# Performance work log

Hardware: AMD Instinct MI355X
Metric: run time of the kernel (lower is better)

## Reference

```python
import jax, jax.numpy as jnp
import numpy as np

N, E, G = 20000, 200000, 32
D, H, C, L = 384, 12, 32, 6
NUM_RBF = 100
RBF_MIN, RBF_MAX = 0.0, 30.0


def _layer_norm(x, g, b, eps=1e-5):
    mu = jnp.mean(x, axis=-1, keepdims=True)
    var = jnp.var(x, axis=-1, keepdims=True)
    return (x - mu) * jax.lax.rsqrt(var + eps) * g + b


def setup_inputs() -> dict:
    key = jax.random.key(0)
    ks = jax.random.split(key, 32)
    s = 0.05
    inp = {
        'x': jax.random.normal(ks[0], (N, 20), jnp.float32),
        'pos': jax.random.normal(ks[1], (N, 3), jnp.float32) * 10.0,
        'edge_index': jax.random.randint(ks[2], (2, E), 0, N),
        'batch': jnp.sort(jax.random.randint(ks[3], (N,), 0, G)),
        # node embedding: Linear(20,384) + LayerNorm
        'emb_W': jax.random.normal(ks[4], (20, D)) * s,
        'emb_b': jnp.zeros((D,)),
        'emb_g': jnp.ones((D,)),
        'emb_beta': jnp.zeros((D,)),
        # edge encoder: Linear(100,384), Linear(384,384), LayerNorm
        'eW1': jax.random.normal(ks[5], (NUM_RBF, D)) * s,
        'eb1': jnp.zeros((D,)),
        'eW2': jax.random.normal(ks[6], (D, D)) * s,
        'eb2': jnp.zeros((D,)),
        'e_g': jnp.ones((D,)),
        'e_beta': jnp.zeros((D,)),
        # 6 stacked GATv2 layers
        'Wl': jax.random.normal(ks[7], (L, D, D)) * s,
        'bl': jnp.zeros((L, D)),
        'Wr': jax.random.normal(ks[8], (L, D, D)) * s,
        'br': jnp.zeros((L, D)),
        'We': jax.random.normal(ks[9], (L, D, D)) * s,
        'att': jax.random.normal(ks[10], (L, H, C)) * s,
        'cb': jnp.zeros((L, D)),
        # BatchNorm (eval mode, running stats)
        'bn_g': 1.0 + jax.random.normal(ks[11], (L, D)) * 0.05,
        'bn_b': jax.random.normal(ks[12], (L, D)) * 0.05,
        'bn_m': jax.random.normal(ks[13], (L, D)) * 0.05,
        'bn_v': jax.random.uniform(ks[14], (L, D), minval=0.5, maxval=1.5),
        # pool combine + head
        'pW': jax.random.normal(ks[15], (2 * D, D)) * s,
        'pb': jnp.zeros((D,)),
        'hW1': jax.random.normal(ks[16], (D, D)) * s,
        'hb1': jnp.zeros((D,)),
        'hW2': jax.random.normal(ks[17], (D, D // 2)) * s,
        'hb2': jnp.zeros((D // 2,)),
        'hW3': jax.random.normal(ks[18], (D // 2, 1)) * s,
        'hb3': jnp.zeros((1,)),
    }
    return inp


def reference(x, pos, edge_index, batch, emb_W, emb_b, emb_g, emb_beta,
              eW1, eb1, eW2, eb2, e_g, e_beta,
              Wl, bl, Wr, br, We, att, cb, bn_g, bn_b, bn_m, bn_v,
              pW, pb, hW1, hb1, hW2, hb2, hW3, hb3):
    src, dst = edge_index[0], edge_index[1]

    # node embedding (dropout = identity in eval)
    h = jax.nn.silu(_layer_norm(x @ emb_W + emb_b, emb_g, emb_beta))  # (N, D)

    # RBF edge features
    centers = jnp.linspace(RBF_MIN, RBF_MAX, NUM_RBF)
    spacing = (RBF_MAX - RBF_MIN) / (NUM_RBF - 1)
    gamma = 1.0 / (spacing ** 2 + 1e-8)
    dist = jnp.linalg.norm(pos[src] - pos[dst], axis=-1, keepdims=True)  # (E, 1)
    rbf = jnp.exp(-gamma * (dist - centers) ** 2)  # (E, NUM_RBF)
    e = jax.nn.silu(rbf @ eW1 + eb1)
    e = _layer_norm(e @ eW2 + eb2, e_g, e_beta)  # (E, D)

    for i in range(L):
        identity = h
        xl = (h @ Wl[i] + bl[i]).reshape(N, H, C)
        xr = (h @ Wr[i] + br[i]).reshape(N, H, C)
        ee = (e @ We[i]).reshape(E, H, C)
        m = jax.nn.leaky_relu(xl[src] + xr[dst] + ee, 0.2)  # (E, H, C)
        logits = jnp.einsum('ehc,hc->eh', m, att[i])  # (E, H)
        smax = jax.ops.segment_max(logits, dst, num_segments=N)
        a = jnp.exp(logits - smax[dst])
        denom = jax.ops.segment_sum(a, dst, num_segments=N)
        a = a / (denom[dst] + 1e-16)
        msg = (xl[src] * a[:, :, None]).reshape(E, H * C)
        out = jax.ops.segment_sum(msg, dst, num_segments=N) + cb[i]  # (N, D)
        out = (out - bn_m[i]) * jax.lax.rsqrt(bn_v[i] + 1e-5) * bn_g[i] + bn_b[i]
        h = jax.nn.silu(out) + identity

    cnt = jax.ops.segment_sum(jnp.ones((N,), h.dtype), batch, num_segments=G)
    h_mean = jax.ops.segment_sum(h, batch, num_segments=G) / jnp.maximum(cnt, 1.0)[:, None]
    h_max = jax.ops.segment_max(h, batch, num_segments=G)
    hg = jnp.concatenate([h_mean, h_max], axis=-1)  # (G, 2D)
    hg = jax.nn.silu(hg @ pW + pb)
    hg = jax.nn.silu(hg @ hW1 + hb1)
    hg = jax.nn.silu(hg @ hW2 + hb2)
    return (hg @ hW3 + hb3).squeeze(-1)  # (G,)
```

## Files before the change

kernel.cpp:

```cpp
#include <hip/hip_runtime.h>
#include <hip/hip_bf16.h>
#include <math.h>

#define NN 20000
#define EE 200000
#define GG 32
#define DD 384
#define HH 12
#define CC 32
#define LL 6
#define NRBF 100
#define CHUNK 32768

typedef short s16x8 __attribute__((ext_vector_type(8)));
typedef float f32x4 __attribute__((ext_vector_type(4)));
typedef unsigned int u32;

__device__ __forceinline__ float siluf(float x) { return x / (1.f + __expf(-x)); }
__device__ __forceinline__ float bf2f(unsigned short u) {
    return __uint_as_float(((unsigned int)u) << 16);
}

__device__ __forceinline__ void atomicMaxF(float* addr, float val) {
    if (val >= 0.f) atomicMax((int*)addr, __float_as_int(val));
    else atomicMin((unsigned int*)addr, __float_as_uint(val));
}

__device__ __forceinline__ void gload16(const void* g, void* l) {
    __builtin_amdgcn_global_load_lds((const __attribute__((address_space(1))) u32*)g,
                                     (__attribute__((address_space(3))) u32*)l, 16, 0, 0);
}

__device__ __forceinline__ bool tile_decode(int NC, int nrows, int& rowt, int& col) {
    const int t = blockIdx.x;
    const int q = t >> 3;
    col = q % NC;
    rowt = (q / NC) * 8 + (t & 7);
    return rowt < nrows;
}

__global__ void EquivariantProteinGNN_45552423141948_kernel() {}

__device__ __forceinline__ void gemm_kloop(const __hip_bfloat16* __restrict__ A,
                                           const __hip_bfloat16* __restrict__ Bt,
                                           int M, int K, int m0, int n0,
                                           unsigned short* As, unsigned short* Bs,
                                           f32x4 (&acc)[4][4]) {
    char* AsB = (char*)As;
    char* BsB = (char*)Bs;
    const int t = threadIdx.x;
    const int w = t >> 6, l = t & 63;
    const int wr = w >> 1, wc = w & 1;

    const int s0 = 4 * w;
    size_t aS[4], bS[4];
#pragma unroll
    for (int i = 0; i < 4; ++i) {
        const int s = s0 + i;
        const int row = s * 8 + (l >> 3);
        const int cg = (l & 7) ^ (row & 7);
        aS[i] = (size_t)min(m0 + row, M - 1) * K + cg * 8;
        bS[i] = (size_t)(n0 + row) * K + cg * 8;
    }

    int aoff[2][4], boff[2][4];
#pragma unroll
    for (int sub = 0; sub < 2; ++sub)
#pragma unroll
        for (int m = 0; m < 4; ++m) {
            const int row = wr * 64 + m * 16 + (l & 15);
            aoff[sub][m] = row * 128 + ((((l >> 4) + 4 * sub) ^ (row & 7)) << 4);
            const int rowb = wc * 64 + m * 16 + (l & 15);
            boff[sub][m] = rowb * 128 + ((((l >> 4) + 4 * sub) ^ (rowb & 7)) << 4);
        }

    for (int kk = 0; kk < K; kk += 64) {
        __syncthreads();
#pragma unroll
        for (int i = 0; i < 4; ++i) gload16(A + aS[i] + kk, As + (s0 + i) * 512);
#pragma unroll
        for (int i = 0; i < 4; ++i) gload16(Bt + bS[i] + kk, Bs + (s0 + i) * 512);
        __syncthreads();
#pragma unroll
        for (int sub = 0; sub < 2; ++sub) {
            s16x8 af[4], bfr[4];
#pragma unroll
            for (int m = 0; m < 4; ++m) af[m] = *(const s16x8*)(AsB + aoff[sub][m]);
#pragma unroll
            for (int n = 0; n < 4; ++n) bfr[n] = *(const s16x8*)(BsB + boff[sub][n]);
#pragma unroll
            for (int m = 0; m < 4; ++m)
#pragma unroll
                for (int n = 0; n < 4; ++n)
                    acc[m][n] = __builtin_amdgcn_mfma_f32_16x16x32_bf16(af[m], bfr[n],
                                                                        acc[m][n], 0, 0, 0);
        }
    }
}

template<bool BIAS, bool SILU>
__global__ __launch_bounds__(256) void k_gemm_bt(const __hip_bfloat16* __restrict__ A,
                                                 const __hip_bfloat16* __restrict__ Bt,
                                                 const float* __restrict__ bias,
                                                 __hip_bfloat16* __restrict__ Cmat,
                                                 int M, int N, int K) {
    int rowt, colt;
    if (!tile_decode(N >> 7, (M + 127) >> 7, rowt, colt)) return;
    const int m0 = rowt << 7, n0 = colt << 7;

    __shared__ unsigned short As[128 * 64];
    __shared__ unsigned short Bs[128 * 64];
    const int l = threadIdx.x & 63;
    const int w = threadIdx.x >> 6;
    const int wr = w >> 1, wc = w & 1;

    f32x4 acc[4][4] = {};
    gemm_kloop(A, Bt, M, K, m0, n0, As, Bs, acc);

#pragma unroll
    for (int n = 0; n < 4; ++n) {
        const int col = n0 + wc * 64 + n * 16 + (l & 15);
        const float bv = BIAS ? bias[col] : 0.f;
#pragma unroll
        for (int m = 0; m < 4; ++m) {
            const int rbase = m0 + wr * 64 + m * 16 + ((l >> 4) << 2);
#pragma unroll
            for (int r = 0; r < 4; ++r) {
                const int row = rbase + r;
                if (row < M) {
                    float v = acc[m][n][r] + bv;
                    if (SILU) v = siluf(v);
                    Cmat[(size_t)row * N + col] = __float2bfloat16(v);
                }
            }
        }
    }
}

__global__ __launch_bounds__(256) void k_gemm_attn(const __hip_bfloat16* __restrict__ A,
                                                   const __hip_bfloat16* __restrict__ Bt,
                                                   const __hip_bfloat16* __restrict__ xlr,
                                                   const int* __restrict__ src_p,
                                                   const int* __restrict__ dst_p,
                                                   const float* __restrict__ att_i,
                                                   float* __restrict__ logits,
                                                   int M, int K) {
    int rowt, colt;
    if (!tile_decode(DD >> 7, (M + 127) >> 7, rowt, colt)) return;
    const int m0 = rowt << 7, n0 = colt << 7;

    __shared__ char smem[32768];
    unsigned short* As = (unsigned short*)smem;
    unsigned short* Bs = (unsigned short*)(smem + 16384);
    const int l = threadIdx.x & 63;
    const int w = threadIdx.x >> 6;
    const int wr = w >> 1, wc = w & 1;

    f32x4 acc[4][4] = {};
    gemm_kloop(A, Bt, M, K, m0, n0, As, Bs, acc);

    __syncthreads();

    float* ep = (float*)(smem + w * 4096);
    const int row_l = l >> 2;
    const int c0 = (l & 3) << 4;
    const int gcol = n0 + wc * 64 + c0;
    const int hbase = (n0 + wc * 64) >> 5;
    const int rswz = row_l << 2;

    float attv[16];
#pragma unroll
    for (int k = 0; k < 4; ++k)
        *(float4*)(attv + 4 * k) = *(const float4*)(att_i + gcol + 4 * k);

#pragma unroll
    for (int m = 0; m < 4; ++m) {
#pragma unroll
        for (int n = 0; n < 4; ++n)
#pragma unroll
            for (int r = 0; r < 4; ++r) {
                const int row = ((l >> 4) << 2) + r;
                const int col = (n << 4) + (l & 15);
                ep[(row << 6) + (col ^ (row << 2))] = acc[m][n][r];
            }
        const int growu = m0 + wr * 64 + m * 16 + row_l;
        const int grow = min(growu, M - 1);
        const int s = src_p[grow], d = dst_p[grow];
        float av[16];
#pragma unroll
        for (int k = 0; k < 4; ++k) {
            const int sc0 = (c0 + (k << 2)) ^ rswz;
            *(f32x4*)(av + 4 * k) = *(const f32x4*)(ep + (row_l << 6) + sc0);
        }
        const uint4 vl0 = *(const uint4*)(xlr + (size_t)s * 768 + gcol);
        const uint4 vl1 = *(const uint4*)(xlr + (size_t)s * 768 + gcol + 8);
        const uint4 vr0 = *(const uint4*)(xlr + (size_t)d * 768 + 384 + gcol);
        const uint4 vr1 = *(const uint4*)(xlr + (size_t)d * 768 + 384 + gcol + 8);
        const u32 lw[8] = {vl0.x, vl0.y, vl0.z, vl0.w, vl1.x, vl1.y, vl1.z, vl1.w};
        const u32 rw[8] = {vr0.x, vr0.y, vr0.z, vr0.w, vr1.x, vr1.y, vr1.z, vr1.w};
        float part = 0.f;
#pragma unroll
        for (int q = 0; q < 8; ++q) {
            float v0 = av[2 * q] + bf2f((unsigned short)(lw[q] & 0xffff)) +
                       bf2f((unsigned short)(rw[q] & 0xffff));
            float v1 = av[2 * q + 1] + bf2f((unsigned short)(lw[q] >> 16)) +
                       bf2f((unsigned short)(rw[q] >> 16));
            v0 = (v0 > 0.f) ? v0 : 0.2f * v0;
            v1 = (v1 > 0.f) ? v1 : 0.2f * v1;
            part += v0 * attv[2 * q] + v1 * attv[2 * q + 1];
        }
        part += __shfl_xor(part, 1, 64);
        if (growu < M && (l & 1) == 0)
            logits[(size_t)growu * HH + hbase + ((l & 2) >> 1)] = part;
    }
}

__global__ void k_tw(const float* __restrict__ in, __hip_bfloat16* __restrict__ out, int nmat) {
    const size_t idx = (size_t)blockIdx.x * 256 + threadIdx.x;
    if (idx >= (size_t)nmat * DD * DD) return;
    const int m = idx / (DD * DD);
    const int rem = idx - (size_t)m * DD * DD;
    const int n = rem / DD, k = rem - n * DD;
    out[idx] = __float2bfloat16(in[(size_t)m * DD * DD + (size_t)k * DD + n]);
}

__global__ void k_twlr(const float* __restrict__ Wl, const float* __restrict__ Wr,
                       __hip_bfloat16* __restrict__ out) {
    const size_t idx = (size_t)blockIdx.x * 256 + threadIdx.x;
    if (idx >= (size_t)LL * 768 * DD) return;
    const int i = idx / (768 * DD);
    const int rem = idx - (size_t)i * 768 * DD;
    const int n = rem / DD, k = rem - n * DD;
    const float v = (n < DD) ? Wl[(size_t)i * DD * DD + (size_t)k * DD + n]
                             : Wr[(size_t)i * DD * DD + (size_t)k * DD + (n - DD)];
    out[idx] = __float2bfloat16(v);
}

__global__ void k_blr(const float* __restrict__ bl, const float* __restrict__ br,
                      float* __restrict__ blr) {
    const int idx = blockIdx.x * 256 + threadIdx.x;
    if (idx >= LL * 768) return;
    const int i = idx / 768, c = idx - i * 768;
    blr[idx] = (c < DD) ? bl[i * DD + c] : br[i * DD + c - DD];
}

__global__ void k_tw1(const float* __restrict__ in, __hip_bfloat16* __restrict__ out) {
    const int idx = blockIdx.x * 256 + threadIdx.x;
    if (idx >= DD * 128) return;
    const int n = idx >> 7, k = idx & 127;
    out[idx] = __float2bfloat16(k < NRBF ? in[(size_t)k * DD + n] : 0.f);
}

__global__ __launch_bounds__(256) void k_rbf_chunk(const float* __restrict__ pos,
                                                   const int* __restrict__ src_p,
                                                   const int* __restrict__ dst_p,
                                                   int e0, int cm,
                                                   __hip_bfloat16* __restrict__ rbfp) {
    const int el = blockIdx.x * 2 + (threadIdx.x >> 7);
    if (el >= cm) return;
    const int e = e0 + el;
    const int c = threadIdx.x & 127;
    const int s = src_p[e], d = dst_p[e];
    const float dx = pos[s * 3 + 0] - pos[d * 3 + 0];
    const float dy = pos[s * 3 + 1] - pos[d * 3 + 1];
    const float dz = pos[s * 3 + 2] - pos[d * 3 + 2];
    const float dist = sqrtf(dx * dx + dy * dy + dz * dz);
    const float spacing = 30.f / 99.f;
    const float gamma = 1.f / (spacing * spacing + 1e-8f);
    float v = 0.f;
    if (c < NRBF) {
        const float dd = dist - (float)c * spacing;
        v = __expf(-gamma * dd * dd);
    }
    rbfp[(size_t)el * 128 + c] = __float2bfloat16(v);
}

__global__ __launch_bounds__(512) void k_ln_rows(__hip_bfloat16* __restrict__ u,
                                                 const float* __restrict__ g,
                                                 const float* __restrict__ be) {
    const int w = threadIdx.x >> 6, l = threadIdx.x & 63;
    const int row = blockIdx.x * 8 + w;
    float vals[8];
    float s = 0.f, q = 0.f;
    if (l < 48) {
        const uint4 vu = *(const uint4*)(u + (size_t)row * DD + 8 * l);
        const unsigned int* uw = (const unsigned int*)&vu;
#pragma unroll
        for (int i = 0; i < 4; ++i) {
            vals[2 * i] = bf2f((unsigned short)(uw[i] & 0xffff));
            vals[2 * i + 1] = bf2f((unsigned short)(uw[i] >> 16));
        }
#pragma unroll
        for (int i = 0; i < 8; ++i) { s += vals[i]; q += vals[i] * vals[i]; }
    }
#pragma unroll
    for (int off = 1; off < 64; off <<= 1) {
        s += __shfl_xor(s, off, 64);
        q += __shfl_xor(q, off, 64);
    }
    const float mu = s / DD;
    const float rs = rsqrtf(q / DD - mu * mu + 1e-5f);
    if (l < 48) {
        unsigned int ow[4];
        const float4 g0 = *(const float4*)(g + 8 * l);
        const float4 g1 = *(const float4*)(g + 8 * l + 4);
        const float4 b0 = *(const float4*)(be + 8 * l);
        const float4 b1 = *(const float4*)(be + 8 * l + 4);
        const float gv[8] = {g0.x, g0.y, g0.z, g0.w, g1.x, g1.y, g1.z, g1.w};
        const float bv[8] = {b0.x, b0.y, b0.z, b0.w, b1.x, b1.y, b1.z, b1.w};
#pragma unroll
        for (int i = 0; i < 4; ++i) {
            const float y0 = (vals[2 * i] - mu) * rs * gv[2 * i] + bv[2 * i];
            const float y1 = (vals[2 * i + 1] - mu) * rs * gv[2 * i + 1] + bv[2 * i + 1];
            const unsigned short h0 = __bfloat16_as_ushort(__float2bfloat16(y0));
            const unsigned short h1 = __bfloat16_as_ushort(__float2bfloat16(y1));
            ow[i] = (unsigned int)h0 | ((unsigned int)h1 << 16);
        }
        *(uint4*)(u + (size_t)row * DD + 8 * l) = *(uint4*)ow;
    }
}

__global__ __launch_bounds__(384) void k_node_embed(const float* __restrict__ x,
                                                    const float* __restrict__ W,
                                                    const float* __restrict__ b,
                                                    const float* __restrict__ g,
                                                    const float* __restrict__ be,
                                                    float* __restrict__ h,
                                                    __hip_bfloat16* __restrict__ hb) {
    const int n = blockIdx.x, j = threadIdx.x;
    __shared__ float xrow[20];
    __shared__ float red[12];
    if (j < 20) xrow[j] = x[n * 20 + j];
    __syncthreads();
    float acc = b[j];
#pragma unroll
    for (int k = 0; k < 20; ++k) acc += xrow[k] * W[k * DD + j];
    float s = acc, q = acc * acc;
#pragma unroll
    for (int off = 32; off > 0; off >>= 1) {
        s += __shfl_down(s, off, 64);
        q += __shfl_down(q, off, 64);
    }
    const int wid = j >> 6;
    if ((j & 63) == 0) { red[wid] = s; red[6 + wid] = q; }
    __syncthreads();
    if (j == 0) {
        float ts = 0.f, tq = 0.f;
        for (int w = 0; w < 6; ++w) { ts += red[w]; tq += red[6 + w]; }
        float mu = ts / DD;
        red[0] = mu; red[6] = tq / DD - mu * mu;
    }
    __syncthreads();
    const float mu = red[0], var = red[6];
    float y = (acc - mu) * rsqrtf(var + 1e-5f) * g[j] + be[j];
    y = siluf(y);
    h[(size_t)n * DD + j] = y;
    hb[(size_t)n * DD + j] = __float2bfloat16(y);
}

__global__ void k_deg(const int* __restrict__ ei, int* __restrict__ deg) {
    int e = blockIdx.x * blockDim.x + threadIdx.x;
    if (e < EE) atomicAdd(&deg[ei[EE + e]], 1);
}

__global__ __launch_bounds__(1024) void k_scan(const int* __restrict__ deg, int* __restrict__ rp) {
    __shared__ int buf[1024];
    __shared__ int carry_s;
    const int tid = threadIdx.x;
    if (tid == 0) carry_s = 0;
    __syncthreads();
    for (int base = 0; base < NN; base += 1024) {
        int v = (base + tid < NN) ? deg[base + tid] : 0;
        buf[tid] = v;
        __syncthreads();
        for (int off = 1; off < 1024; off <<= 1) {
            int t = (tid >= off) ? buf[tid - off] : 0;
            __syncthreads();
            buf[tid] += t;
            __syncthreads();
        }
        const int incl = buf[tid];
        const int carry = carry_s;
        if (base + tid < NN) rp[base + tid] = carry + incl - v;
        __syncthreads();
        if (tid == 1023) carry_s = carry + incl;
        __syncthreads();
    }
    if (tid == 0) rp[NN] = carry_s;
}

__global__ void k_scatter(const int* __restrict__ ei, const int* __restrict__ rp,
                          int* __restrict__ cursor, int* __restrict__ col_e) {
    int e = blockIdx.x * blockDim.x + threadIdx.x;
    if (e < EE) {
        int d = ei[EE + e];
        int p = atomicAdd(&cursor[d], 1);
        col_e[rp[d] + p] = e;
    }
}

__global__ void k_perm(const int* __restrict__ ei, const int* __restrict__ col_e,
                       int* __restrict__ src_p, int* __restrict__ dst_p) {
    int p = blockIdx.x * blockDim.x + threadIdx.x;
    if (p < EE) {
        const int e = col_e[p];
        src_p[p] = ei[e];
        dst_p[p] = ei[EE + e];
    }
}

__global__ __launch_bounds__(256) void k_node_aggr(const float* __restrict__ logits,
                                                   const __hip_bfloat16* __restrict__ xlr,
                                                   const int* __restrict__ src_p,
                                                   const int* __restrict__ rp,
                                                   const float* __restrict__ cb_i,
                                                   const float* __restrict__ g_i,
                                                   const float* __restrict__ b_i,
                                                   const float* __restrict__ m_i,
                                                   const float* __restrict__ v_i,
                                                   float* __restrict__ h,
                                                   __hip_bfloat16* __restrict__ hb) {
    const int wv = threadIdx.x >> 6, l = threadIdx.x & 63;
    const int n = blockIdx.x * 4 + wv;
    if (n >= NN) return;
    const int beg = rp[n], end = rp[n + 1];

    float mx = -INFINITY, sum = 0.f;
    if (l < HH) {
        for (int i = beg; i < end; ++i) mx = fmaxf(mx, logits[(size_t)i * HH + l]);
        for (int i = beg; i < end; ++i) sum += __expf(logits[(size_t)i * HH + l] - mx);
    }
    const int head = (l < 48) ? (l >> 2) : 0;
    const float m_h = __shfl(mx, head, 64);
    const float inv_h = 1.f / (__shfl(sum, head, 64) + 1e-16f);

    if (l >= 48) return;
    const int c0 = l * 8;
    float acc[8] = {};
    for (int i = beg; i < end; ++i) {
        const float a = __expf(logits[(size_t)i * HH + head] - m_h) * inv_h;
        const int s = src_p[i];
        const uint4 vx = *(const uint4*)(xlr + (size_t)s * 768 + c0);
        const u32* xw = (const u32*)&vx;
#pragma unroll
        for (int q = 0; q < 4; ++q) {
            acc[2 * q]     += bf2f((unsigned short)(xw[q] & 0xffff)) * a;
            acc[2 * q + 1] += bf2f((unsigned short)(xw[q] >> 16)) * a;
        }
    }
    const float4 cb0 = *(const float4*)(cb_i + c0), cb1 = *(const float4*)(cb_i + c0 + 4);
    const float4 gg0 = *(const float4*)(g_i + c0),  gg1 = *(const float4*)(g_i + c0 + 4);
    const float4 bb0 = *(const float4*)(b_i + c0),  bb1 = *(const float4*)(b_i + c0 + 4);
    const float4 mm0 = *(const float4*)(m_i + c0),  mm1 = *(const float4*)(m_i + c0 + 4);
    const float4 vv0 = *(const float4*)(v_i + c0),  vv1 = *(const float4*)(v_i + c0 + 4);
    const float cbv[8] = {cb0.x, cb0.y, cb0.z, cb0.w, cb1.x, cb1.y, cb1.z, cb1.w};
    const float gv[8]  = {gg0.x, gg0.y, gg0.z, gg0.w, gg1.x, gg1.y, gg1.z, gg1.w};
    const float bv[8]  = {bb0.x, bb0.y, bb0.z, bb0.w, bb1.x, bb1.y, bb1.z, bb1.w};
    const float mv[8]  = {mm0.x, mm0.y, mm0.z, mm0.w, mm1.x, mm1.y, mm1.z, mm1.w};
    const float vvv[8] = {vv0.x, vv0.y, vv0.z, vv0.w, vv1.x, vv1.y, vv1.z, vv1.w};
    float4 h0 = *(const float4*)(h + (size_t)n * DD + c0);
    float4 h1 = *(const float4*)(h + (size_t)n * DD + c0 + 4);
    float hv[8] = {h0.x, h0.y, h0.z, h0.w, h1.x, h1.y, h1.z, h1.w};
    unsigned int ow[4];
#pragma unroll
    for (int q = 0; q < 8; ++q) {
        float o = acc[q] + cbv[q];
        o = (o - mv[q]) * rsqrtf(vvv[q] + 1e-5f) * gv[q] + bv[q];
        hv[q] = siluf(o) + hv[q];
    }
#pragma unroll
    for (int q = 0; q < 4; ++q) {
        const unsigned short b0 = __bfloat16_as_ushort(__float2bfloat16(hv[2 * q]));
        const unsigned short b1 = __bfloat16_as_ushort(__float2bfloat16(hv[2 * q + 1]));
        ow[q] = (unsigned int)b0 | ((unsigned int)b1 << 16);
    }
    *(float4*)(h + (size_t)n * DD + c0) = make_float4(hv[0], hv[1], hv[2], hv[3]);
    *(float4*)(h + (size_t)n * DD + c0 + 4) = make_float4(hv[4], hv[5], hv[6], hv[7]);
    *(uint4*)(hb + (size_t)n * DD + c0) = *(uint4*)ow;
}

__global__ void k_fill(float* __restrict__ p, float v, int n) {
    int i = blockIdx.x * blockDim.x + threadIdx.x;
    if (i < n) p[i] = v;
}

__global__ __launch_bounds__(384) void k_pool2(const float* __restrict__ h,
                                               const int* __restrict__ batch,
                                               float* __restrict__ gsum,
                                               float* __restrict__ gmax,
                                               float* __restrict__ gcnt) {
    const int j = threadIdx.x;
    const int n0 = blockIdx.x * 256;
    const int n1 = min(n0 + 256, NN);
    int cur = batch[n0];
    float s = 0.f, mx = -INFINITY;
    int cnt = 0;
    for (int n = n0; n < n1; ++n) {
        const int g = batch[n];
        if (g != cur) {
            atomicAdd(&gsum[cur * DD + j], s);
            atomicMaxF(&gmax[cur * DD + j], mx);
            if (j == 0) atomicAdd(&gcnt[cur], (float)cnt);
            s = 0.f; mx = -INFINITY; cnt = 0; cur = g;
        }
        const float v = h[(size_t)n * DD + j];
        s += v; mx = fmaxf(mx, v); ++cnt;
    }
    atomicAdd(&gsum[cur * DD + j], s);
    atomicMaxF(&gmax[cur * DD + j], mx);
    if (j == 0) atomicAdd(&gcnt[cur], (float)cnt);
}

__global__ __launch_bounds__(384) void k_head(const float* __restrict__ gsum,
                                              const float* __restrict__ gmax,
                                              const float* __restrict__ gcnt,
                                              const float* __restrict__ pW,
                                              const float* __restrict__ pb,
                                              const float* __restrict__ hW1,
                                              const float* __restrict__ hb1,
                                              const float* __restrict__ hW2,
                                              const float* __restrict__ hb2,
                                              const float* __restrict__ hW3,
                                              const float* __restrict__ hb3,
                                              float* __restrict__ out) {
    const int g = blockIdx.x, j = threadIdx.x;
    __shared__ float hg[2 * DD];
    __shared__ float p1[DD];
    __shared__ float p2[DD];
    __shared__ float p3[DD / 2];
    __shared__ float red[6];
    const float cnt = fmaxf(gcnt[g], 1.f);
    hg[j] = gsum[g * DD + j] / cnt;
    hg[DD + j] = gmax[g * DD + j];
    __syncthreads();
    float a = pb[j];
    for (int k = 0; k < 2 * DD; ++k) a += hg[k] * pW[(size_t)k * DD + j];
    p1[j] = siluf(a);
    __syncthreads();
    a = hb1[j];
    for (int k = 0; k < DD; ++k) a += p1[k] * hW1[(size_t)k * DD + j];
    p2[j] = siluf(a);
    __syncthreads();
    if (j < DD / 2) {
        a = hb2[j];
        for (int k = 0; k < DD; ++k) a += p2[k] * hW2[(size_t)k * (DD / 2) + j];
        p3[j] = siluf(a);
    }
    __syncthreads();
    float v = (j < DD / 2) ? p3[j] * hW3[j] : 0.f;
#pragma unroll
    for (int off = 32; off > 0; off >>= 1) v += __shfl_down(v, off, 64);
    if ((j & 63) == 0) red[j >> 6] = v;
    __syncthreads();
    if (j == 0) {
        float s = 0.f;
        for (int w = 0; w < 6; ++w) s += red[w];
        out[g] = s + hb3[0];
    }
}

static inline int gemm_grid(int M, int N) {
    const int nr = (M + 127) >> 7, nc = N >> 7;
    return ((nr + 7) >> 3) * nc * 8;
}

extern "C" void kernel_launch(void* const* d_in, const int* in_sizes, int n_in,
                              void* d_out, int out_size, void* d_ws, size_t ws_size,
                              hipStream_t stream) {
    (void)in_sizes; (void)n_in; (void)out_size; (void)ws_size;
    const float* x      = (const float*)d_in[0];
    const float* pos    = (const float*)d_in[1];
    const int*   ei     = (const int*)d_in[2];
    const int*   batch  = (const int*)d_in[3];
    const float* emb_W  = (const float*)d_in[4];
    const float* emb_b  = (const float*)d_in[5];
    const float* emb_g  = (const float*)d_in[6];
    const float* emb_be = (const float*)d_in[7];
    const float* eW1    = (const float*)d_in[8];
    const float* eb1    = (const float*)d_in[9];
    const float* eW2    = (const float*)d_in[10];
    const float* eb2    = (const float*)d_in[11];
    const float* e_g    = (const float*)d_in[12];
    const float* e_be   = (const float*)d_in[13];
    const float* Wl     = (const float*)d_in[14];
    const float* bl     = (const float*)d_in[15];
    const float* Wr     = (const float*)d_in[16];
    const float* br     = (const float*)d_in[17];
    const float* We     = (const float*)d_in[18];
    const float* att    = (const float*)d_in[19];
    const float* cb     = (const float*)d_in[20];
    const float* bn_g   = (const float*)d_in[21];
    const float* bn_b   = (const float*)d_in[22];
    const float* bn_m   = (const float*)d_in[23];
    const float* bn_v   = (const float*)d_in[24];
    const float* pW     = (const float*)d_in[25];
    const float* pb     = (const float*)d_in[26];
    const float* hW1    = (const float*)d_in[27];
    const float* hb1    = (const float*)d_in[28];
    const float* hW2    = (const float*)d_in[29];
    const float* hb2    = (const float*)d_in[30];
    const float* hW3    = (const float*)d_in[31];
    const float* hb3    = (const float*)d_in[32];

    char* wp = (char*)d_ws;
    auto carve = [&](size_t bytes) -> void* {
        void* p = (void*)wp;
        wp += (bytes + 255) & ~(size_t)255;
        return p;
    };
    float* h      = (float*)carve((size_t)NN * DD * 4);
    __hip_bfloat16* hbf = (__hip_bfloat16*)carve((size_t)NN * DD * 2);
    __hip_bfloat16* xlr = (__hip_bfloat16*)carve((size_t)NN * 768 * 2);
    __hip_bfloat16* ebf = (__hip_bfloat16*)carve((size_t)EE * DD * 2);
    float* logits = (float*)carve((size_t)EE * HH * 4);
    int* deg      = (int*)carve((size_t)NN * 4);
    int* cursor   = (int*)carve((size_t)NN * 4);
    int* rp       = (int*)carve((size_t)(NN + 1) * 4);
    int* col_e    = (int*)carve((size_t)EE * 4);
    int* src_p    = (int*)carve((size_t)EE * 4);
    int* dst_p    = (int*)carve((size_t)EE * 4);
    float* gsum   = (float*)carve((size_t)GG * DD * 4);
    float* gmax   = (float*)carve((size_t)GG * DD * 4);
    float* gcnt   = (float*)carve((size_t)GG * 4);
    __hip_bfloat16* Wlrt = (__hip_bfloat16*)carve((size_t)LL * 768 * DD * 2);
    __hip_bfloat16* Wet  = (__hip_bfloat16*)carve((size_t)LL * DD * DD * 2);
    float* blr    = (float*)carve((size_t)LL * 768 * 4);
    __hip_bfloat16* eW1t = (__hip_bfloat16*)carve((size_t)DD * 128 * 2);
    __hip_bfloat16* eW2t = (__hip_bfloat16*)carve((size_t)DD * DD * 2);

    __hip_bfloat16* rbfc = (__hip_bfloat16*)logits;
    __hip_bfloat16* tc   = xlr;

    hipMemsetAsync(deg, 0, (size_t)NN * 4, stream);
    hipMemsetAsync(cursor, 0, (size_t)NN * 4, stream);

    {
        const int nblkLR = (int)(((size_t)LL * 768 * DD + 255) / 256);
        const int nblk6 = (int)(((size_t)LL * DD * DD + 255) / 256);
        k_twlr<<<nblkLR, 256, 0, stream>>>(Wl, Wr, Wlrt);
        k_tw<<<nblk6, 256, 0, stream>>>(We, Wet, LL);
        k_blr<<<(LL * 768 + 255) / 256, 256, 0, stream>>>(bl, br, blr);
        k_tw<<<(DD * DD + 255) / 256, 256, 0, stream>>>(eW2, eW2t, 1);
        k_tw1<<<(DD * 128 + 255) / 256, 256, 0, stream>>>(eW1, eW1t);
    }

    k_node_embed<<<NN, 384, 0, stream>>>(x, emb_W, emb_b, emb_g, emb_be, h, hbf);

    k_deg<<<(EE + 255) / 256, 256, 0, stream>>>(ei, deg);
    k_scan<<<1, 1024, 0, stream>>>(deg, rp);
    k_scatter<<<(EE + 255) / 256, 256, 0, stream>>>(ei, rp, cursor, col_e);
    k_perm<<<(EE + 255) / 256, 256, 0, stream>>>(ei, col_e, src_p, dst_p);

    for (int c0 = 0; c0 < EE; c0 += CHUNK) {
        const int cm = (EE - c0 < CHUNK) ? (EE - c0) : CHUNK;
        k_rbf_chunk<<<(cm + 1) / 2, 256, 0, stream>>>(pos, src_p, dst_p, c0, cm, rbfc);
        k_gemm_bt<true, true><<<gemm_grid(cm, DD), 256, 0, stream>>>(rbfc, eW1t, eb1, tc, cm, DD, 128);
        k_gemm_bt<true, false><<<gemm_grid(cm, DD), 256, 0, stream>>>(tc, eW2t, eb2,
                                                                      ebf + (size_t)c0 * DD, cm, DD, DD);
    }
    k_ln_rows<<<EE / 8, 512, 0, stream>>>(ebf, e_g, e_be);

    for (int i = 0; i < LL; ++i) {
        const __hip_bfloat16* Wlrt_i = Wlrt + (size_t)i * 768 * DD;
        const __hip_bfloat16* Wet_i  = Wet + (size_t)i * DD * DD;
        const float* blr_i = blr + (size_t)i * 768;
        const float* att_i = att + (size_t)i * HH * CC;
        const float* cb_i  = cb + (size_t)i * DD;
        const float* bng_i = bn_g + (size_t)i * DD;
        const float* bnb_i = bn_b + (size_t)i * DD;
        const float* bnm_i = bn_m + (size_t)i * DD;
        const float* bnv_i = bn_v + (size_t)i * DD;

        k_gemm_bt<true, false><<<gemm_grid(NN, 768), 256, 0, stream>>>(hbf, Wlrt_i, blr_i, xlr,
                                                                       NN, 768, DD);
        k_gemm_attn<<<gemm_grid(EE, DD), 256, 0, stream>>>(ebf, Wet_i, xlr, src_p, dst_p,
                                                           att_i, logits, EE, DD);
        k_node_aggr<<<(NN + 3) / 4, 256, 0, stream>>>(logits, xlr, src_p, rp, cb_i, bng_i, bnb_i,
                                                      bnm_i, bnv_i, h, hbf);
    }

    hipMemsetAsync(gsum, 0, (size_t)GG * DD * 4, stream);
    hipMemsetAsync(gcnt, 0, (size_t)GG * 4, stream);
    k_fill<<<(GG * DD + 255) / 256, 256, 0, stream>>>(gmax, -INFINITY, GG * DD);
    k_pool2<<<(NN + 255) / 256, 384, 0, stream>>>(h, batch, gsum, gmax, gcnt);
    k_head<<<GG, 384, 0, stream>>>(gsum, gmax, gcnt, pW, pb, hW1, hb1, hW2, hb2, hW3, hb3,
                                   (float*)d_out);
}
```

Baseline: 1.884 ms.

## Halve GEMM K-tile to 32 with new LDS swizzle and hoist epilogue gathers

Shrinks the per-block LDS tiles from 128x64 to 128x32 bf16, with a matching XOR swizzle and one MFMA sub-step per iteration. This halves shared memory use, which can allow more resident blocks. In the attention-fused GEMM, the src/dst index and xl/xr gather loads are issued before the LDS transpose to hide their latency. The trade-off is twice as many barrier-separated K iterations, with less work per sync.

```diff
diff --git a/kernel.cpp b/kernel.cpp
--- a/kernel.cpp
+++ b/kernel.cpp
@@ -52,49 +52,46 @@
     const int w = t >> 6, l = t & 63;
     const int wr = w >> 1, wc = w & 1;
 
-    const int s0 = 4 * w;
-    size_t aS[4], bS[4];
-#pragma unroll
-    for (int i = 0; i < 4; ++i) {
-        const int s = s0 + i;
-        const int row = s * 8 + (l >> 3);
-        const int cg = (l & 7) ^ (row & 7);
-        aS[i] = (size_t)min(m0 + row, M - 1) * K + cg * 8;
-        bS[i] = (size_t)(n0 + row) * K + cg * 8;
-    }
-
-    int aoff[2][4], boff[2][4];
-#pragma unroll
-    for (int sub = 0; sub < 2; ++sub)
-#pragma unroll
-        for (int m = 0; m < 4; ++m) {
-            const int row = wr * 64 + m * 16 + (l & 15);
-            aoff[sub][m] = row * 128 + ((((l >> 4) + 4 * sub) ^ (row & 7)) << 4);
-            const int rowb = wc * 64 + m * 16 + (l & 15);
-            boff[sub][m] = rowb * 128 + ((((l >> 4) + 4 * sub) ^ (rowb & 7)) << 4);
-        }
-
-    for (int kk = 0; kk < K; kk += 64) {
+    const int seg0 = 2 * w, seg1 = seg0 + 1;
+    const int r0s = seg0 * 16 + (l >> 2);
+    const int r1s = seg1 * 16 + (l >> 2);
+    const int cg0 = (l & 3) ^ ((r0s >> 1) & 3);
+    const int cg1 = (l & 3) ^ ((r1s >> 1) & 3);
+    const size_t aSrc0 = (size_t)min(m0 + r0s, M - 1) * K + cg0 * 8;
+    const size_t aSrc1 = (size_t)min(m0 + r1s, M - 1) * K + cg1 * 8;
+    const size_t bSrc0 = (size_t)(n0 + r0s) * K + cg0 * 8;
+    const size_t bSrc1 = (size_t)(n0 + r1s) * K + cg1 * 8;
+    unsigned short* AsW0 = As + seg0 * 512;
+    unsigned short* AsW1 = As + seg1 * 512;
+    unsigned short* BsW0 = Bs + seg0 * 512;
+    unsigned short* BsW1 = Bs + seg1 * 512;
+
+    int aoff[4], boff[4];
+#pragma unroll
+    for (int m = 0; m < 4; ++m) {
+        const int row = wr * 64 + m * 16 + (l & 15);
+        aoff[m] = row * 64 + ((((l >> 4)) ^ ((row >> 1) & 3)) << 4);
+        const int rowb = wc * 64 + m * 16 + (l & 15);
+        boff[m] = rowb * 64 + ((((l >> 4)) ^ ((rowb >> 1) & 3)) << 4);
+    }
+
+    for (int kk = 0; kk < K; kk += 32) {
         __syncthreads();
-#pragma unroll
-        for (int i = 0; i < 4; ++i) gload16(A + aS[i] + kk, As + (s0 + i) * 512);
-#pragma unroll
-        for (int i = 0; i < 4; ++i) gload16(Bt + bS[i] + kk, Bs + (s0 + i) * 512);
+        gload16(A + aSrc0 + kk, AsW0);
+        gload16(A + aSrc1 + kk, AsW1);
+        gload16(Bt + bSrc0 + kk, BsW0);
+        gload16(Bt + bSrc1 + kk, BsW1);
         __syncthreads();
-#pragma unroll
-        for (int sub = 0; sub < 2; ++sub) {
-            s16x8 af[4], bfr[4];
-#pragma unroll
-            for (int m = 0; m < 4; ++m) af[m] = *(const s16x8*)(AsB + aoff[sub][m]);
-#pragma unroll
-            for (int n = 0; n < 4; ++n) bfr[n] = *(const s16x8*)(BsB + boff[sub][n]);
-#pragma unroll
-            for (int m = 0; m < 4; ++m)
-#pragma unroll
-                for (int n = 0; n < 4; ++n)
-                    acc[m][n] = __builtin_amdgcn_mfma_f32_16x16x32_bf16(af[m], bfr[n],
-                                                                        acc[m][n], 0, 0, 0);
-        }
+        s16x8 af[4], bfr[4];
+#pragma unroll
+        for (int m = 0; m < 4; ++m) af[m] = *(const s16x8*)(AsB + aoff[m]);
+#pragma unroll
+        for (int n = 0; n < 4; ++n) bfr[n] = *(const s16x8*)(BsB + boff[n]);
+#pragma unroll
+        for (int m = 0; m < 4; ++m)
+#pragma unroll
+            for (int n = 0; n < 4; ++n)
+                acc[m][n] = __builtin_amdgcn_mfma_f32_16x16x32_bf16(af[m], bfr[n], acc[m][n], 0, 0, 0);
     }
 }
 
@@ -108,8 +105,8 @@
     if (!tile_decode(N >> 7, (M + 127) >> 7, rowt, colt)) return;
     const int m0 = rowt << 7, n0 = colt << 7;
 
-    __shared__ unsigned short As[128 * 64];
-    __shared__ unsigned short Bs[128 * 64];
+    __shared__ unsigned short As[128 * 32];
+    __shared__ unsigned short Bs[128 * 32];
     const int l = threadIdx.x & 63;
     const int w = threadIdx.x >> 6;
     const int wr = w >> 1, wc = w & 1;
@@ -149,9 +146,9 @@
     if (!tile_decode(DD >> 7, (M + 127) >> 7, rowt, colt)) return;
     const int m0 = rowt << 7, n0 = colt << 7;
 
-    __shared__ char smem[32768];
+    __shared__ char smem[16384];
     unsigned short* As = (unsigned short*)smem;
-    unsigned short* Bs = (unsigned short*)(smem + 16384);
+    unsigned short* Bs = (unsigned short*)(smem + 8192);
     const int l = threadIdx.x & 63;
     const int w = threadIdx.x >> 6;
     const int wr = w >> 1, wc = w & 1;
@@ -175,6 +172,14 @@
 
 #pragma unroll
     for (int m = 0; m < 4; ++m) {
+        const int growu = m0 + wr * 64 + m * 16 + row_l;
+        const int grow = min(growu, M - 1);
+        const int s = src_p[grow], d = dst_p[grow];
+        const uint4 vl0 = *(const uint4*)(xlr + (size_t)s * 768 + gcol);
+        const uint4 vl1 = *(const uint4*)(xlr + (size_t)s * 768 + gcol + 8);
+        const uint4 vr0 = *(const uint4*)(xlr + (size_t)d * 768 + 384 + gcol);
+        const uint4 vr1 = *(const uint4*)(xlr + (size_t)d * 768 + 384 + gcol + 8);
+
 #pragma unroll
         for (int n = 0; n < 4; ++n)
 #pragma unroll
@@ -183,19 +188,12 @@
                 const int col = (n << 4) + (l & 15);
                 ep[(row << 6) + (col ^ (row << 2))] = acc[m][n][r];
             }
-        const int growu = m0 + wr * 64 + m * 16 + row_l;
-        const int grow = min(growu, M - 1);
-        const int s = src_p[grow], d = dst_p[grow];
         float av[16];
 #pragma unroll
         for (int k = 0; k < 4; ++k) {
             const int sc0 = (c0 + (k << 2)) ^ rswz;
             *(f32x4*)(av + 4 * k) = *(const f32x4*)(ep + (row_l << 6) + sc0);
         }
-        const uint4 vl0 = *(const uint4*)(xlr + (size_t)s * 768 + gcol);
-        const uint4 vl1 = *(const uint4*)(xlr + (size_t)s * 768 + gcol + 8);
-        const uint4 vr0 = *(const uint4*)(xlr + (size_t)d * 768 + 384 + gcol);
-        const uint4 vr1 = *(const uint4*)(xlr + (size_t)d * 768 + 384 + gcol + 8);
         const u32 lw[8] = {vl0.x, vl0.y, vl0.z, vl0.w, vl1.x, vl1.y, vl1.z, vl1.w};
         const u32 rw[8] = {vr0.x, vr0.y, vr0.z, vr0.w, vr1.x, vr1.y, vr1.z, vr1.w};
         float part = 0.f;
```

After: 1.897 ms. Within noise of the previous version (+0.7%).
